# Optimization experiments

Hardware: AMD Instinct MI355X
Metric: run time of the kernel (lower is better)

The kernel has to match this reference:

```python
import jax, jax.numpy as jnp
import numpy as np

D_MODEL = 1024
N_HEAD = 16
D_HEAD = D_MODEL // N_HEAD


def setup_inputs() -> dict:
    key = jax.random.key(0)
    ks = jax.random.split(key, 12)
    L, B, M = 2048, 2, 2048
    s = 1.0 / np.sqrt(D_MODEL)
    return {
        "q": jax.random.normal(ks[0], (L, B, D_MODEL), jnp.float32),
        "kv": jax.random.normal(ks[1], (L, B, D_MODEL), jnp.float32),
        "mem": jax.random.normal(ks[2], (M, B, D_MODEL), jnp.float32),
        "w_q": jax.random.normal(ks[3], (D_MODEL, D_MODEL), jnp.float32) * s,
        "b_q": jnp.zeros((D_MODEL,), jnp.float32),
        "w_k": jax.random.normal(ks[4], (D_MODEL, D_MODEL), jnp.float32) * s,
        "b_k": jnp.zeros((D_MODEL,), jnp.float32),
        "w_v": jax.random.normal(ks[5], (D_MODEL, D_MODEL), jnp.float32) * s,
        "b_v": jnp.zeros((D_MODEL,), jnp.float32),
        "w_c": jax.random.normal(ks[6], (D_MODEL, D_MODEL), jnp.float32) * s,
        "b_c": jnp.zeros((D_MODEL,), jnp.float32),
    }


def reference(q, kv, mem, w_q, b_q, w_k, b_k, w_v, b_v, w_c, b_c):
    # c: [L+M, B, D]
    c = jnp.concatenate([mem, kv], axis=0)
    L, B, _ = q.shape
    J = c.shape[0]
    # linear projections (torch Linear: x @ W^T + b)
    qh = (q @ w_q.T + b_q).reshape(L, B, N_HEAD, D_HEAD)
    kh = (c @ w_k.T + b_k).reshape(J, B, N_HEAD, D_HEAD)
    vh = (c @ w_v.T + b_v).reshape(J, B, N_HEAD, D_HEAD)
    # attention scores [i, j, b, n]
    score = jnp.einsum("ibnd,jbnd->ijbn", qh, kh) / np.sqrt(D_HEAD).astype(np.float32)
    prob = jax.nn.softmax(score, axis=1)
    vec = jnp.einsum("ijbn,jbnd->ibnd", prob, vh).reshape(L, B, D_MODEL)
    return vec @ w_c.T + b_c
```

## Files before the change

### kernel.cpp

```cpp
#include <hip/hip_runtime.h>


using short8 = __attribute__((ext_vector_type(8))) short;
using f32x4  = __attribute__((ext_vector_type(4))) float;

#define DEV __device__ __forceinline__

DEV unsigned short f2bf(float f) {
  union { float f; unsigned int u; } x; x.f = f;
  unsigned int r = x.u + 0x7FFFu + ((x.u >> 16) & 1u);
  return (unsigned short)(r >> 16);
}

DEV unsigned int cvtpk(float lo, float hi) {
  unsigned int r;
  asm("v_cvt_pk_bf16_f32 %0, %1, %2" : "=v"(r) : "v"(lo), "v"(hi));
  return r;
}

DEV float max3f(float a, float b, float c) {
  float d;
  asm("v_max3_f32 %0, %1, %2, %3" : "=v"(d) : "v"(a), "v"(b), "v"(c));
  return d;
}

DEV void gload_lds16(const unsigned short* g, unsigned short* l) {
  __builtin_amdgcn_global_load_lds(
      (const __attribute__((address_space(1))) unsigned int*)g,
      (__attribute__((address_space(3))) unsigned int*)l, 16, 0, 0);
}

#define BARRIER_RAW()                      \
  do {                                     \
    __builtin_amdgcn_sched_barrier(0);     \
    __builtin_amdgcn_s_barrier();          \
    __builtin_amdgcn_sched_barrier(0);     \
  } while (0)

__global__ __launch_bounds__(256) void convert_all(
    const float* __restrict__ q, const float* __restrict__ mem_,
    const float* __restrict__ kv, const float* __restrict__ wq,
    const float* __restrict__ wk, const float* __restrict__ wv,
    const float* __restrict__ wc, unsigned short* __restrict__ a_bf,
    unsigned short* __restrict__ c_bf, unsigned short* __restrict__ w_bf) {
  size_t u = (size_t)blockIdx.x * 256 + threadIdx.x;
  const float* src;
  unsigned short* dst;
  if (u < 524288u)        { src = q    + u * 8;                dst = a_bf + u * 8; }
  else if (u < 1048576u)  { src = mem_ + (u - 524288u) * 8;    dst = c_bf + (u - 524288u) * 8; }
  else if (u < 1572864u)  { src = kv   + (u - 1048576u) * 8;   dst = c_bf + 4194304u + (u - 1048576u) * 8; }
  else if (u < 1703936u)  { src = wq   + (u - 1572864u) * 8;   dst = w_bf + (u - 1572864u) * 8; }
  else if (u < 1835008u)  { src = wk   + (u - 1703936u) * 8;   dst = w_bf + 1048576u + (u - 1703936u) * 8; }
  else if (u < 1966080u)  { src = wv   + (u - 1835008u) * 8;   dst = w_bf + 2097152u + (u - 1835008u) * 8; }
  else                    { src = wc   + (u - 1966080u) * 8;   dst = w_bf + 3145728u + (u - 1966080u) * 8; }
  float4 v0 = ((const float4*)src)[0];
  float4 v1 = ((const float4*)src)[1];
  union { unsigned short us[8]; uint4 v; } o;
  o.us[0] = f2bf(v0.x); o.us[1] = f2bf(v0.y); o.us[2] = f2bf(v0.z); o.us[3] = f2bf(v0.w);
  o.us[4] = f2bf(v1.x); o.us[5] = f2bf(v1.y); o.us[6] = f2bf(v1.z); o.us[7] = f2bf(v1.w);
  *(uint4*)dst = o.v;
}

template <int MODE>
__global__ __launch_bounds__(256, 2) void gemm_bt(
    const unsigned short* __restrict__ A, const unsigned short* __restrict__ Bw,
    const float* __restrict__ bias, void* __restrict__ outp) {
  __shared__ __align__(16) unsigned short lA[128 * 64];
  __shared__ __align__(16) unsigned short lB[128 * 64];
  const int tid = threadIdx.x;
  const int lane = tid & 63;
  const int w = tid >> 6;
  const int wr = w >> 1, wcn = w & 1;
  const int tm = blockIdx.x * 128;
  const int tn = blockIdx.y * 128;

  const int srow = lane >> 3;
  const int scol = ((lane & 7) ^ srow) * 8;
  const unsigned short* aptr = A + (size_t)(tm + 32 * w + srow) * 1024 + scol;
  const unsigned short* bptr = Bw + (size_t)(tn + 32 * w + srow) * 1024 + scol;
  unsigned short* lAw = &lA[(32 * w) * 64];
  unsigned short* lBw = &lB[(32 * w) * 64];

  const f32x4 zero = {0.f, 0.f, 0.f, 0.f};
  f32x4 acc[4][4];
#pragma unroll
  for (int i = 0; i < 4; ++i)
#pragma unroll
    for (int j = 0; j < 4; ++j) acc[i][j] = zero;

  for (int kb = 0; kb < 16; ++kb) {
    const int ko = kb * 64;
#pragma unroll
    for (int c = 0; c < 4; ++c) {
      gload_lds16(aptr + ko + c * 8 * 1024, lAw + c * 8 * 64);
      gload_lds16(bptr + ko + c * 8 * 1024, lBw + c * 8 * 64);
    }
    __syncthreads();
#pragma unroll
    for (int kk = 0; kk < 2; ++kk) {
      short8 af[4], bfr[4];
#pragma unroll
      for (int mi = 0; mi < 4; ++mi) {
        int r = 64 * wr + 16 * mi + (lane & 15);
        int slot = (kk * 4 + (lane >> 4)) ^ (r & 7);
        af[mi] = *(const short8*)&lA[r * 64 + slot * 8];
      }
#pragma unroll
      for (int ni = 0; ni < 4; ++ni) {
        int r = 64 * wcn + 16 * ni + (lane & 15);
        int slot = (kk * 4 + (lane >> 4)) ^ (r & 7);
        bfr[ni] = *(const short8*)&lB[r * 64 + slot * 8];
      }
#pragma unroll
      for (int mi = 0; mi < 4; ++mi)
#pragma unroll
        for (int ni = 0; ni < 4; ++ni)
          acc[mi][ni] = __builtin_amdgcn_mfma_f32_16x16x32_bf16(
              af[mi], bfr[ni], acc[mi][ni], 0, 0, 0);
    }
    __syncthreads();
  }

  const int g4 = (lane >> 4) * 4;
  const int c0 = lane & 15;
#pragma unroll
  for (int mi = 0; mi < 4; ++mi) {
#pragma unroll
    for (int ni = 0; ni < 4; ++ni) {
      const int colt = tn + 64 * wcn + 16 * ni + c0;
      const float bv = bias[colt];
#pragma unroll
      for (int j = 0; j < 4; ++j) {
        const int rowt = tm + 64 * wr + 16 * mi + g4 + j;
        const float v = acc[mi][ni][j] + bv;
        if constexpr (MODE == 0) {
          ((float*)outp)[(size_t)rowt * 1024 + colt] = v;
        } else {
          const int i = rowt >> 1, b = rowt & 1, n = colt >> 6, d = colt & 63;
          ((unsigned short*)outp)[(((size_t)(b * 16 + n) * 2048 + i) << 6) + d] =
              f2bf(v * 0.1803368801111f);
        }
      }
    }
  }
}

__global__ __launch_bounds__(256, 2) void gemm_kv(
    const unsigned short* __restrict__ A, const unsigned short* __restrict__ wk,
    const unsigned short* __restrict__ wv, const float* __restrict__ bk,
    const float* __restrict__ bv, unsigned short* __restrict__ ko,
    unsigned short* __restrict__ vo) {
  __shared__ __align__(16) unsigned short lA[128 * 64];
  __shared__ __align__(16) unsigned short lB[128 * 64];
  const int tid = threadIdx.x;
  const int lane = tid & 63;
  const int w = tid >> 6;
  const int wr = w >> 1, wcn = w & 1;
  const int tm = blockIdx.x * 128;
  const int yy = blockIdx.y;
  const bool isV = yy >= 8;
  const int tn = (yy & 7) * 128;
  const unsigned short* Bw = isV ? wv : wk;
  const float* bias = isV ? bv : bk;

  const int srow = lane >> 3;
  const int scol = ((lane & 7) ^ srow) * 8;
  const unsigned short* aptr = A + (size_t)(tm + 32 * w + srow) * 1024 + scol;
  const unsigned short* bptr = Bw + (size_t)(tn + 32 * w + srow) * 1024 + scol;
  unsigned short* lAw = &lA[(32 * w) * 64];
  unsigned short* lBw = &lB[(32 * w) * 64];

  const f32x4 zero = {0.f, 0.f, 0.f, 0.f};
  f32x4 acc[4][4];
#pragma unroll
  for (int i = 0; i < 4; ++i)
#pragma unroll
    for (int j = 0; j < 4; ++j) acc[i][j] = zero;

  for (int kb = 0; kb < 16; ++kb) {
    const int ko_ = kb * 64;
#pragma unroll
    for (int c = 0; c < 4; ++c) {
      gload_lds16(aptr + ko_ + c * 8 * 1024, lAw + c * 8 * 64);
      gload_lds16(bptr + ko_ + c * 8 * 1024, lBw + c * 8 * 64);
    }
    __syncthreads();
#pragma unroll
    for (int kk = 0; kk < 2; ++kk) {
      short8 af[4], bfr[4];
#pragma unroll
      for (int mi = 0; mi < 4; ++mi) {
        int r = 64 * wr + 16 * mi + (lane & 15);
        int slot = (kk * 4 + (lane >> 4)) ^ (r & 7);
        af[mi] = *(const short8*)&lA[r * 64 + slot * 8];
      }
#pragma unroll
      for (int ni = 0; ni < 4; ++ni) {
        int r = 64 * wcn + 16 * ni + (lane & 15);
        int slot = (kk * 4 + (lane >> 4)) ^ (r & 7);
        bfr[ni] = *(const short8*)&lB[r * 64 + slot * 8];
      }
#pragma unroll
      for (int mi = 0; mi < 4; ++mi)
#pragma unroll
        for (int ni = 0; ni < 4; ++ni)
          acc[mi][ni] = __builtin_amdgcn_mfma_f32_16x16x32_bf16(
              af[mi], bfr[ni], acc[mi][ni], 0, 0, 0);
    }
    __syncthreads();
  }

  const int g4 = (lane >> 4) * 4;
  const int c0 = lane & 15;
#pragma unroll
  for (int mi = 0; mi < 4; ++mi) {
#pragma unroll
    for (int ni = 0; ni < 4; ++ni) {
      const int colt = tn + 64 * wcn + 16 * ni + c0;
      const float bvv = bias[colt];
#pragma unroll
      for (int j = 0; j < 4; ++j) {
        const int rowt = tm + 64 * wr + 16 * mi + g4 + j;
        const float v = acc[mi][ni][j] + bvv;
        const int jj = rowt >> 1, b = rowt & 1, n = colt >> 6, d = colt & 63;
        if (!isV) {
          ko[(((size_t)(b * 16 + n) * 4096 + jj) << 6) + d] = f2bf(v);
        } else {
          const int j6 = jj & 63;
          const int pos = (j6 & 3) | (((j6 >> 4) & 1) << 2) | (((j6 >> 2) & 3) << 3) |
                          (((j6 >> 5) & 1) << 5);
          vo[((size_t)(b * 16 + n) * 64 + d) * 4096 + (jj & ~63) + pos] = f2bf(v);
        }
      }
    }
  }
}

__global__ __launch_bounds__(256, 2) void attn_kernel(
    const unsigned short* __restrict__ qh, const unsigned short* __restrict__ kh,
    const unsigned short* __restrict__ vt, unsigned short* __restrict__ vec) {
  __shared__ __align__(16) unsigned short kl[2][2][64 * 64];
  __shared__ __align__(16) unsigned short vl[2][2][64 * 64];
  const int tid = threadIdx.x;
  const int lane = tid & 63;
  const int w = tid >> 6;
  const int g = lane >> 4;
  const int l4 = lane & 15;
  const int f = blockIdx.x;
  const int head = (f & 7) * 4 + ((f >> 3) & 3);
  const int qt = f >> 5;
  const int b = head >> 4, n = head & 15;
  const unsigned short* qbase = qh + ((size_t)head * 2048 + qt * 128 + 32 * w) * 64;
  const unsigned short* kbase = kh + (size_t)head * 4096 * 64;
  const unsigned short* vbase = vt + (size_t)head * 64 * 4096;

  short8 qf[2][2];
#pragma unroll
  for (int mi = 0; mi < 2; ++mi)
#pragma unroll
    for (int kk = 0; kk < 2; ++kk)
      qf[mi][kk] = *(const short8*)&qbase[(16 * mi + l4) * 64 + kk * 32 + g * 8];

  const f32x4 zero = {0.f, 0.f, 0.f, 0.f};
  f32x4 oacc[2][4];
#pragma unroll
  for (int mi = 0; mi < 2; ++mi)
#pragma unroll
    for (int nd = 0; nd < 4; ++nd) oacc[mi][nd] = zero;
  float mrow[2] = {-3.0e38f, -3.0e38f};
  float lsum[2] = {0.f, 0.f};

  const int srow = lane >> 3;
  const int scol = ((lane & 7) ^ srow) * 8;
  const unsigned short* kp = kbase + (size_t)(16 * w + srow) * 64 + scol;
  const unsigned short* vp = vbase + (size_t)(16 * w + srow) * 4096 + scol;

  auto stage_pair = [&](int jp, int bufi) {
#pragma unroll
    for (int sub = 0; sub < 2; ++sub) {
      gload_lds16(kp + (size_t)jp * 8192 + sub * 4096,
                  &kl[bufi][sub][(16 * w) * 64]);
      gload_lds16(kp + (size_t)jp * 8192 + sub * 4096 + 8 * 64,
                  &kl[bufi][sub][(16 * w + 8) * 64]);
      gload_lds16(vp + jp * 128 + sub * 64, &vl[bufi][sub][(16 * w) * 64]);
      gload_lds16(vp + jp * 128 + sub * 64 + 8 * 4096,
                  &vl[bufi][sub][(16 * w + 8) * 64]);
    }
  };

  auto qkt = [&](const unsigned short* kbuf, f32x4 (&s)[2][4]) {
#pragma unroll
    for (int mi = 0; mi < 2; ++mi)
#pragma unroll
      for (int nj = 0; nj < 4; ++nj) s[mi][nj] = zero;
    __builtin_amdgcn_s_setprio(1);
#pragma unroll
    for (int kk = 0; kk < 2; ++kk) {
      short8 bk[4];
#pragma unroll
      for (int nj = 0; nj < 4; ++nj) {
        int r = 16 * nj + l4;
        int slot = (kk * 4 + g) ^ (r & 7);
        bk[nj] = *(const short8*)&kbuf[r * 64 + slot * 8];
      }
#pragma unroll
      for (int mi = 0; mi < 2; ++mi)
#pragma unroll
        for (int nj = 0; nj < 4; ++nj)
          s[mi][nj] = __builtin_amdgcn_mfma_f32_16x16x32_bf16(bk[nj], qf[mi][kk], s[mi][nj], 0, 0, 0);
    }
    __builtin_amdgcn_s_setprio(0);
  };

  auto sm = [&](f32x4 (&s)[2][4], short8 (&pa)[2][2]) {
    float pm[2];
#pragma unroll
    for (int mi = 0; mi < 2; ++mi) {
      float t0 = max3f(s[mi][0][0], s[mi][0][1], s[mi][0][2]);
      float t1 = max3f(s[mi][0][3], s[mi][1][0], s[mi][1][1]);
      float t2 = max3f(s[mi][1][2], s[mi][1][3], s[mi][2][0]);
      float t3 = max3f(s[mi][2][1], s[mi][2][2], s[mi][2][3]);
      float t4 = max3f(s[mi][3][0], s[mi][3][1], s[mi][3][2]);
      float p5 = max3f(t0, t1, t2);
      p5 = max3f(p5, t3, t4);
      pm[mi] = fmaxf(p5, s[mi][3][3]);
    }
    float pj = fmaxf(pm[0], pm[1]);
    pj = fmaxf(pj, __shfl_xor(pj, 16));
    pj = fmaxf(pj, __shfl_xor(pj, 32));
    if (!__all(pj <= fminf(mrow[0], mrow[1]) + 8.f)) {
#pragma unroll
      for (int mi = 0; mi < 2; ++mi) {
        const float mnew = fmaxf(mrow[mi], pj);
        const float sc = __builtin_amdgcn_exp2f(mrow[mi] - mnew);
        mrow[mi] = mnew;
        lsum[mi] *= sc;
#pragma unroll
        for (int reg = 0; reg < 4; ++reg) {
          const float scr = __shfl(sc, 4 * g + reg);
#pragma unroll
          for (int nd = 0; nd < 4; ++nd) oacc[mi][nd][reg] *= scr;
        }
      }
    }
#pragma unroll
    for (int mi = 0; mi < 2; ++mi) {
      const float m = mrow[mi];
      float tr[4];
#pragma unroll
      for (int nj = 0; nj < 4; ++nj) {
        const float p0 = __builtin_amdgcn_exp2f(s[mi][nj][0] - m);
        const float p1 = __builtin_amdgcn_exp2f(s[mi][nj][1] - m);
        const float p2 = __builtin_amdgcn_exp2f(s[mi][nj][2] - m);
        const float p3 = __builtin_amdgcn_exp2f(s[mi][nj][3] - m);
        s[mi][nj][0] = p0; s[mi][nj][1] = p1; s[mi][nj][2] = p2; s[mi][nj][3] = p3;
        tr[nj] = (p0 + p1) + (p2 + p3);
      }
      lsum[mi] += (tr[0] + tr[1]) + (tr[2] + tr[3]);
#pragma unroll
      for (int kk2 = 0; kk2 < 2; ++kk2) {
        union { unsigned int u[4]; short8 v; } t;
#pragma unroll
        for (int wd = 0; wd < 4; ++wd) {
          const int nj = (wd >> 1) + 2 * kk2;
          const int r0 = (wd & 1) * 2;
          t.u[wd] = cvtpk(s[mi][nj][r0], s[mi][nj][r0 + 1]);
        }
        pa[mi][kk2] = t.v;
      }
    }
  };

  auto pv = [&](const short8 (&pa)[2][2], const unsigned short* vbuf) {
    __builtin_amdgcn_s_setprio(1);
#pragma unroll
    for (int kk2 = 0; kk2 < 2; ++kk2) {
      short8 bv4[4];
#pragma unroll
      for (int nd = 0; nd < 4; ++nd) {
        const int r = 16 * nd + l4;
        const int blk = (g + 4 * kk2) ^ (r & 7);
        bv4[nd] = *(const short8*)&vbuf[r * 64 + blk * 8];
      }
#pragma unroll
      for (int mi = 0; mi < 2; ++mi)
#pragma unroll
        for (int nd = 0; nd < 4; ++nd)
          oacc[mi][nd] = __builtin_amdgcn_mfma_f32_16x16x32_bf16(pa[mi][kk2], bv4[nd], oacc[mi][nd], 0, 0, 0);
    }
    __builtin_amdgcn_s_setprio(0);
  };

  f32x4 sA[2][4], sB[2][4];
  short8 paA[2][2], paB[2][2];
  auto pair = [&](int bufi) {
    qkt(kl[bufi][0], sA);
    qkt(kl[bufi][1], sB);
    sm(sA, paA);
    pv(paA, vl[bufi][0]);
    sm(sB, paB);
    pv(paB, vl[bufi][1]);
  };

  stage_pair(0, 0);
  asm volatile("s_waitcnt vmcnt(0)" ::: "memory");
  BARRIER_RAW();

  for (int t2 = 0; t2 < 16; ++t2) {
    stage_pair(2 * t2 + 1, 1);
    pair(0);
    asm volatile("s_waitcnt vmcnt(0)" ::: "memory");
    BARRIER_RAW();
    if (t2 < 15) stage_pair(2 * t2 + 2, 0);
    pair(1);
    if (t2 < 15) {
      asm volatile("s_waitcnt vmcnt(0)" ::: "memory");
      BARRIER_RAW();
    }
  }

#pragma unroll
  for (int mi = 0; mi < 2; ++mi) {
    float l = lsum[mi];
    l += __shfl_xor(l, 16);
    l += __shfl_xor(l, 32);
#pragma unroll
    for (int reg = 0; reg < 4; ++reg) {
      const float lr = __shfl(l, 4 * g + reg);
      const float inv = 1.f / lr;
      const int i = qt * 128 + 32 * w + 16 * mi + 4 * g + reg;
#pragma unroll
      for (int nd = 0; nd < 4; ++nd) {
        const int d = 16 * nd + l4;
        vec[(size_t)(i * 2 + b) * 1024 + n * 64 + d] = f2bf(oacc[mi][nd][reg] * inv);
      }
    }
  }
}

extern "C" void kernel_launch(void* const* d_in, const int* in_sizes, int n_in,
                              void* d_out, int out_size, void* d_ws, size_t ws_size,
                              hipStream_t stream) {
  (void)in_sizes; (void)n_in; (void)out_size; (void)ws_size;
  const float* q    = (const float*)d_in[0];
  const float* kv   = (const float*)d_in[1];
  const float* mem_ = (const float*)d_in[2];
  const float* wq   = (const float*)d_in[3];
  const float* bq   = (const float*)d_in[4];
  const float* wk   = (const float*)d_in[5];
  const float* bk   = (const float*)d_in[6];
  const float* wv   = (const float*)d_in[7];
  const float* bv   = (const float*)d_in[8];
  const float* wc   = (const float*)d_in[9];
  const float* bc   = (const float*)d_in[10];

  char* ws = (char*)d_ws;
  unsigned short* w_bf = (unsigned short*)(ws);
  unsigned short* a_bf = (unsigned short*)(ws + (8ull << 20));
  unsigned short* c_bf = (unsigned short*)(ws + (16ull << 20));
  unsigned short* qhb  = (unsigned short*)(ws + (32ull << 20));
  unsigned short* khb  = (unsigned short*)(ws + (40ull << 20));
  unsigned short* vtb  = (unsigned short*)(ws + (56ull << 20));
  unsigned short* vecb = a_bf;

  convert_all<<<8192, 256, 0, stream>>>(q, mem_, kv, wq, wk, wv, wc, a_bf, c_bf, w_bf);
  gemm_bt<1><<<dim3(32, 8), 256, 0, stream>>>(a_bf, w_bf, bq, qhb);
  gemm_kv<<<dim3(64, 16), 256, 0, stream>>>(c_bf, w_bf + (1u << 20), w_bf + (2u << 20),
                                            bk, bv, khb, vtb);
  attn_kernel<<<512, 256, 0, stream>>>(qhb, khb, vtb, vecb);
  gemm_bt<0><<<dim3(32, 8), 256, 0, stream>>>(vecb, w_bf + (3u << 20), bc, d_out);
}
```

Measured before the change: 180.9 us.

## Load K fragments directly into registers instead of staging through LDS

K tiles are no longer copied into shared memory. Each wave now loads its MFMA K fragments straight from global memory into registers, double-buffered one subtile ahead, while V is still staged through LDS. This halves LDS use and removes the K LDS reads and their bank-swizzle arithmetic. In exchange, all four waves redundantly fetch the same K tile from global/L2, and the register buffers raise VGPR pressure under the 2-blocks-per-CU launch bound.

```diff
diff --git a/kernel.cpp b/kernel.cpp
--- a/kernel.cpp
+++ b/kernel.cpp
@@ -239,7 +239,6 @@
 __global__ __launch_bounds__(256, 2) void attn_kernel(
     const unsigned short* __restrict__ qh, const unsigned short* __restrict__ kh,
     const unsigned short* __restrict__ vt, unsigned short* __restrict__ vec) {
-  __shared__ __align__(16) unsigned short kl[2][2][64 * 64];
   __shared__ __align__(16) unsigned short vl[2][2][64 * 64];
   const int tid = threadIdx.x;
   const int lane = tid & 63;
@@ -272,47 +271,44 @@
 
   const int srow = lane >> 3;
   const int scol = ((lane & 7) ^ srow) * 8;
-  const unsigned short* kp = kbase + (size_t)(16 * w + srow) * 64 + scol;
   const unsigned short* vp = vbase + (size_t)(16 * w + srow) * 4096 + scol;
-
-  auto stage_pair = [&](int jp, int bufi) {
+  const unsigned short* kfrag = kbase + (size_t)l4 * 64 + g * 8;
+
+  auto stage_pairV = [&](int jp, int bufi) {
 #pragma unroll
     for (int sub = 0; sub < 2; ++sub) {
-      gload_lds16(kp + (size_t)jp * 8192 + sub * 4096,
-                  &kl[bufi][sub][(16 * w) * 64]);
-      gload_lds16(kp + (size_t)jp * 8192 + sub * 4096 + 8 * 64,
-                  &kl[bufi][sub][(16 * w + 8) * 64]);
       gload_lds16(vp + jp * 128 + sub * 64, &vl[bufi][sub][(16 * w) * 64]);
       gload_lds16(vp + jp * 128 + sub * 64 + 8 * 4096,
                   &vl[bufi][sub][(16 * w + 8) * 64]);
     }
   };
 
-  auto qkt = [&](const unsigned short* kbuf, f32x4 (&s)[2][4]) {
+  auto kload = [&](int jt, short8 (&kr)[2][4]) {
+    const unsigned short* p = kfrag + (size_t)jt * 4096;
+#pragma unroll
+    for (int kk = 0; kk < 2; ++kk)
+#pragma unroll
+      for (int nj = 0; nj < 4; ++nj)
+        kr[kk][nj] = *(const short8*)&p[nj * 1024 + kk * 32];
+  };
+
+  auto subtile = [&](const short8 (&kr)[2][4], const unsigned short* vbuf) {
+    f32x4 s[2][4];
 #pragma unroll
     for (int mi = 0; mi < 2; ++mi)
 #pragma unroll
       for (int nj = 0; nj < 4; ++nj) s[mi][nj] = zero;
     __builtin_amdgcn_s_setprio(1);
 #pragma unroll
-    for (int kk = 0; kk < 2; ++kk) {
-      short8 bk[4];
-#pragma unroll
-      for (int nj = 0; nj < 4; ++nj) {
-        int r = 16 * nj + l4;
-        int slot = (kk * 4 + g) ^ (r & 7);
-        bk[nj] = *(const short8*)&kbuf[r * 64 + slot * 8];
-      }
+    for (int kk = 0; kk < 2; ++kk)
 #pragma unroll
       for (int mi = 0; mi < 2; ++mi)
 #pragma unroll
         for (int nj = 0; nj < 4; ++nj)
-          s[mi][nj] = __builtin_amdgcn_mfma_f32_16x16x32_bf16(bk[nj], qf[mi][kk], s[mi][nj], 0, 0, 0);
-    }
+          s[mi][nj] = __builtin_amdgcn_mfma_f32_16x16x32_bf16(
+              kr[kk][nj], qf[mi][kk], s[mi][nj], 0, 0, 0);
     __builtin_amdgcn_s_setprio(0);
-  };
-
-  auto sm = [&](f32x4 (&s)[2][4], short8 (&pa)[2][2]) {
+
     float pm[2];
 #pragma unroll
     for (int mi = 0; mi < 2; ++mi) {
@@ -343,6 +339,7 @@
         }
       }
     }
+    short8 pa[2][2];
 #pragma unroll
     for (int mi = 0; mi < 2; ++mi) {
       const float m = mrow[mi];
@@ -369,9 +366,7 @@
         pa[mi][kk2] = t.v;
       }
     }
-  };
-
-  auto pv = [&](const short8 (&pa)[2][2], const unsigned short* vbuf) {
+
     __builtin_amdgcn_s_setprio(1);
 #pragma unroll
     for (int kk2 = 0; kk2 < 2; ++kk2) {
@@ -386,33 +381,32 @@
       for (int mi = 0; mi < 2; ++mi)
 #pragma unroll
         for (int nd = 0; nd < 4; ++nd)
-          oacc[mi][nd] = __builtin_amdgcn_mfma_f32_16x16x32_bf16(pa[mi][kk2], bv4[nd], oacc[mi][nd], 0, 0, 0);
+          oacc[mi][nd] = __builtin_amdgcn_mfma_f32_16x16x32_bf16(
+              pa[mi][kk2], bv4[nd], oacc[mi][nd], 0, 0, 0);
     }
     __builtin_amdgcn_s_setprio(0);
   };
 
-  f32x4 sA[2][4], sB[2][4];
-  short8 paA[2][2], paB[2][2];
-  auto pair = [&](int bufi) {
-    qkt(kl[bufi][0], sA);
-    qkt(kl[bufi][1], sB);
-    sm(sA, paA);
-    pv(paA, vl[bufi][0]);
-    sm(sB, paB);
-    pv(paB, vl[bufi][1]);
-  };
-
-  stage_pair(0, 0);
+  short8 krA[2][4], krB[2][4];
+
+  stage_pairV(0, 0);
+  kload(0, krA);
   asm volatile("s_waitcnt vmcnt(0)" ::: "memory");
   BARRIER_RAW();
 
   for (int t2 = 0; t2 < 16; ++t2) {
-    stage_pair(2 * t2 + 1, 1);
-    pair(0);
+    stage_pairV(2 * t2 + 1, 1);
+    kload(4 * t2 + 1, krB);
+    subtile(krA, vl[0][0]);
+    kload(4 * t2 + 2, krA);
+    subtile(krB, vl[0][1]);
     asm volatile("s_waitcnt vmcnt(0)" ::: "memory");
     BARRIER_RAW();
-    if (t2 < 15) stage_pair(2 * t2 + 2, 0);
-    pair(1);
+    if (t2 < 15) stage_pairV(2 * t2 + 2, 0);
+    kload(4 * t2 + 3, krB);
+    subtile(krA, vl[1][0]);
+    if (t2 < 15) kload(4 * t2 + 4, krA);
+    subtile(krB, vl[1][1]);
     if (t2 < 15) {
       asm volatile("s_waitcnt vmcnt(0)" ::: "memory");
       BARRIER_RAW();
```

After: 231.2 us. 27.8% more time.
